# Performance work log

Measured on AMD Instinct MI355X. Metric: run time of the kernel, lower is better.

## Reference

```python
import jax, jax.numpy as jnp
import numpy as np
import math

HID = 512
HEADS = 8
DK = HID // HEADS
B, S, T = 8, 4096, 512


def setup_inputs() -> dict:
    key = jax.random.key(0)
    ks = jax.random.split(key, 12)
    scale = 0.02
    inp = {
        "inputs": jax.random.normal(ks[0], (B, S, HID), dtype=jnp.float32),
        "targets": jax.random.normal(ks[1], (B, T, HID), dtype=jnp.float32),
        "mask": jnp.ones((B, S), dtype=bool),
        "Wq": jax.random.normal(ks[2], (HID, HID), dtype=jnp.float32) * scale,
        "bq": jnp.zeros((HID,), dtype=jnp.float32),
        "Wk": jax.random.normal(ks[3], (HID, HID), dtype=jnp.float32) * scale,
        "bk": jnp.zeros((HID,), dtype=jnp.float32),
        "Wv": jax.random.normal(ks[4], (HID, HID), dtype=jnp.float32) * scale,
        "bv": jnp.zeros((HID,), dtype=jnp.float32),
        "Wo": jax.random.normal(ks[5], (HID, HID), dtype=jnp.float32) * scale,
        "bo": jnp.zeros((HID,), dtype=jnp.float32),
    }
    return inp


def reference(inputs, targets, mask, Wq, bq, Wk, bk, Wv, bv, Wo, bo):
    # PoolingFunction(method='multihead-attention'), dropout=0 (identity),
    # hidden_size == output_size so mapping_function is identity.
    b, t, h = targets.shape
    s = inputs.shape[1]
    Q = (targets @ Wq.T + bq).reshape(b, t, HEADS, DK)
    K = (inputs @ Wk.T + bk).reshape(b, s, HEADS, DK)
    V = (inputs @ Wv.T + bv).reshape(b, s, HEADS, DK)
    # scores: b x heads x tgt x seq (same math as (Q*K).sum(-1)/sqrt(d_k))
    e = jnp.einsum('bthd,bshd->bhts', Q, K) / math.sqrt(DK)
    neg = (1.0 - mask.astype(jnp.float32)) * -1e20  # b x s
    e = e + neg[:, None, None, :]
    a = jax.nn.softmax(e, axis=-1)  # softmax over seq dim
    ctx = jnp.einsum('bhts,bshd->bthd', a, V).reshape(b, t, h)
    return ctx @ Wo.T + bo
```

## Files before the change

### kernel.cpp

```cpp
#include <hip/hip_runtime.h>
#include <hip/hip_bf16.h>
#include <cstdint>
#include <cstddef>

#define HIDN   512
#define NHEADS 8
#define BATCH  8
#define SLEN   4096
#define TLEN   512
#define SSPLIT 4
#define SCHUNK (SLEN / SSPLIT)
#define SCL2   0.18033688f

typedef __attribute__((ext_vector_type(8))) short   bf16x8;
typedef __attribute__((ext_vector_type(4))) float   f32x4;
typedef unsigned short u16;
typedef unsigned int   u32;

__device__ __forceinline__ u32 pkbf(float a, float b) {
    __hip_bfloat162 h = __float22bfloat162_rn(float2{a, b});
    union { __hip_bfloat162 h; u32 u; } un; un.h = h; return un.u;
}
__device__ __forceinline__ u32 cvtpk(float a, float b) {
    u32 r;
    asm("v_cvt_pk_bf16_f32 %0, %1, %2" : "=v"(r) : "v"(a), "v"(b));
    return r;
}
__device__ __forceinline__ float fexp2(float x) {
    return __builtin_amdgcn_exp2f(x);
}
__device__ __forceinline__ void gload_lds16(const u16* g, u16* l) {
    __builtin_amdgcn_global_load_lds(
        (const __attribute__((address_space(1))) u32*)g,
        (__attribute__((address_space(3))) u32*)l, 16, 0, 0);
}

__global__ __launch_bounds__(256) void cvt_all(
    const float* __restrict__ X, const float* __restrict__ Tg,
    const float* __restrict__ Wq, const float* __restrict__ Wk,
    const float* __restrict__ Wv, const float* __restrict__ Wo,
    const int* __restrict__ mask,
    u16* __restrict__ Xc, u16* __restrict__ Tc, u16* __restrict__ Wc,
    float* __restrict__ negf)
{
    int i4 = blockIdx.x * 256 + threadIdx.x;
    if (i4 >= 4980736) {
        int off = i4 - 4980736;
        int4 mv = ((const int4*)mask)[off];
        float4 nv;
        nv.x = mv.x ? 0.f : -1e30f; nv.y = mv.y ? 0.f : -1e30f;
        nv.z = mv.z ? 0.f : -1e30f; nv.w = mv.w ? 0.f : -1e30f;
        ((float4*)negf)[off] = nv;
        return;
    }
    const float* s; u16* d; long off;
    if (i4 < 4194304)      { s = X;  d = Xc; off = i4; }
    else if (i4 < 4718592) { s = Tg; d = Tc; off = i4 - 4194304; }
    else {
        int wi = i4 - 4718592; int widx = wi >> 16;
        s = (widx == 0) ? Wq : (widx == 1) ? Wk : (widx == 2) ? Wv : Wo;
        d = Wc + widx * 262144; off = wi & 65535;
    }
    float4 v = *(const float4*)(s + off * 4);
    uint2 o; o.x = pkbf(v.x, v.y); o.y = pkbf(v.z, v.w);
    *(uint2*)(d + off * 4) = o;
}

#define GEMM_PIPE_DECLS                                                      \
    const int xg = (qd ^ (m & 3)) * 8;                                       \
    const int f0 = tid, f1 = tid + 256;                                      \
    const int r0r = f0 >> 2, r0c = ((f0 & 3) ^ (r0r & 3)) * 8;               \
    const int r1r = f1 >> 2, r1c = ((f1 & 3) ^ (r1r & 3)) * 8;               \
    const int r0b = (f0 & ~63) * 8, r1b = (f1 & ~63) * 8

#define GSTAGE(Aptr, Bptr, k0, bb) do {                                      \
        gload_lds16(Aptr + (size_t)(m0 + r0r) * HIDN + (k0) + r0c,           \
                    &As[bb][0] + r0b);                                       \
        gload_lds16(Bptr + (size_t)(n0 + r0r) * HIDN + (k0) + r0c,           \
                    &Bs[bb][0] + r0b);                                       \
        gload_lds16(Aptr + (size_t)(m0 + r1r) * HIDN + (k0) + r1c,           \
                    &As[bb][0] + r1b);                                       \
        gload_lds16(Bptr + (size_t)(n0 + r1r) * HIDN + (k0) + r1c,           \
                    &Bs[bb][0] + r1b);                                       \
    } while (0)

#define GCOMP(bb) do {                                                       \
        bf16x8 af[4], bf[4];                                                 \
        _Pragma("unroll")                                                    \
        for (int t = 0; t < 4; ++t) {                                        \
            af[t] = *(bf16x8*)&As[bb][(64 * wm + 16 * t + m) * 32 + xg];     \
            bf[t] = *(bf16x8*)&Bs[bb][(64 * wn + 16 * t + m) * 32 + xg];     \
        }                                                                    \
        _Pragma("unroll")                                                    \
        for (int ti = 0; ti < 4; ++ti)                                       \
            _Pragma("unroll")                                                \
            for (int tj = 0; tj < 4; ++tj)                                   \
                acc[ti][tj] = __builtin_amdgcn_mfma_f32_16x16x32_bf16(       \
                    af[ti], bf[tj], acc[ti][tj], 0, 0, 0);                   \
    } while (0)

#define GEMM_PIPE_LOOP(Aptr, Bptr) do {                                      \
        GSTAGE(Aptr, Bptr, 0, 0);                                            \
        _Pragma("unroll 1")                                                  \
        for (int c = 0; c < (HIDN / 32) - 1; ++c) {                          \
            GSTAGE(Aptr, Bptr, (c + 1) * 32, (c + 1) & 1);                   \
            asm volatile("s_waitcnt vmcnt(4)" ::: "memory");                 \
            __builtin_amdgcn_s_barrier();                                    \
            __builtin_amdgcn_sched_barrier(0);                               \
            GCOMP(c & 1);                                                    \
            __builtin_amdgcn_s_barrier();                                    \
            __builtin_amdgcn_sched_barrier(0);                               \
        }                                                                    \
        asm volatile("s_waitcnt vmcnt(0)" ::: "memory");                     \
        __builtin_amdgcn_s_barrier();                                        \
        __builtin_amdgcn_sched_barrier(0);                                   \
        GCOMP(((HIDN / 32) - 1) & 1);                                        \
    } while (0)

template<int MODE, int SEQ>
__global__ __launch_bounds__(256)
void gemm_bf16(const u16* __restrict__ A, const u16* __restrict__ Bw,
               const float* __restrict__ bias, void* __restrict__ Yv)
{
    __shared__ u16 As[2][128 * 32];
    __shared__ u16 Bs[2][128 * 32];
    const int tid = threadIdx.x;
    const int lane = tid & 63, w = tid >> 6;
    const int m = lane & 15, qd = lane >> 4;
    const int wm = w >> 1, wn = w & 1;
    const int m0 = blockIdx.y * 128, n0 = blockIdx.x * 128;
    GEMM_PIPE_DECLS;

    f32x4 acc[4][4];
#pragma unroll
    for (int i = 0; i < 4; ++i)
#pragma unroll
        for (int j = 0; j < 4; ++j) acc[i][j] = (f32x4){0.f, 0.f, 0.f, 0.f};

    GEMM_PIPE_LOOP(A, Bw);

#pragma unroll
    for (int ti = 0; ti < 4; ++ti) {
        const int gr0 = m0 + 64 * wm + 16 * ti + 4 * qd;
#pragma unroll
        for (int tj = 0; tj < 4; ++tj) {
            const int gcol = n0 + 64 * wn + 16 * tj + m;
            const float bv = bias[gcol];
            if (MODE == 0) {
                float* Y = (float*)Yv;
#pragma unroll
                for (int i = 0; i < 4; ++i)
                    Y[(size_t)(gr0 + i) * HIDN + gcol] = acc[ti][tj][i] + bv;
            } else {
                u16* Y = (u16*)Yv;
                const int b = gr0 / SEQ, h = gcol >> 6, d = gcol & 63;
                const int r = gr0 & (SEQ - 1);
                uint2 o;
                o.x = pkbf(acc[ti][tj][0] + bv, acc[ti][tj][1] + bv);
                o.y = pkbf(acc[ti][tj][2] + bv, acc[ti][tj][3] + bv);
                *(uint2*)&Y[(((size_t)(b * 8 + h)) * 64 + d) * SEQ + r] = o;
            }
        }
    }
}

template<int SEQ>
__global__ __launch_bounds__(256)
void gemm_wxT(const u16* __restrict__ Wm, const u16* __restrict__ X,
              const float* __restrict__ bias, u16* __restrict__ Y)
{
    __shared__ u16 As[2][128 * 32];
    __shared__ u16 Bs[2][128 * 32];
    const int tid = threadIdx.x;
    const int lane = tid & 63, w = tid >> 6;
    const int m = lane & 15, qd = lane >> 4;
    const int wm = w >> 1, wn = w & 1;
    const int m0 = blockIdx.y * 128, n0 = blockIdx.x * 128;
    GEMM_PIPE_DECLS;

    f32x4 acc[4][4];
#pragma unroll
    for (int i = 0; i < 4; ++i)
#pragma unroll
        for (int j = 0; j < 4; ++j) acc[i][j] = (f32x4){0.f, 0.f, 0.f, 0.f};

    GEMM_PIPE_LOOP(Wm, X);

#pragma unroll
    for (int ti = 0; ti < 4; ++ti) {
        const int o = m0 + 64 * wm + 16 * ti + 4 * qd;
        const float4 bv = *(const float4*)&bias[o];
        const int h = o >> 6, d0 = o & 63;
#pragma unroll
        for (int tj = 0; tj < 4; ++tj) {
            const int n = n0 + 64 * wn + 16 * tj + m;
            const int b = n / SEQ, r = n & (SEQ - 1);
            uint2 pk;
            pk.x = pkbf(acc[ti][tj][0] + bv.x, acc[ti][tj][1] + bv.y);
            pk.y = pkbf(acc[ti][tj][2] + bv.z, acc[ti][tj][3] + bv.w);
            *(uint2*)&Y[(((size_t)(b * 8 + h)) * SEQ + r) * 64 + d0] = pk;
        }
    }
}

__global__ __launch_bounds__(256, 2)
void attn_part(const u16* __restrict__ Q, const u16* __restrict__ K,
               const u16* __restrict__ Vt, const float* __restrict__ negf,
               float* __restrict__ Opart, float* __restrict__ lpart)
{
    __shared__ char Psh[32768];
    __shared__ u16  KVl[2][8192];
    __shared__ float Ngl[1024];
    const int tid = threadIdx.x;
    const int lane = tid & 63, w = tid >> 6;
    const int m = lane & 15, qd = lane >> 4;
    const int ti = blockIdx.x, si = blockIdx.y, bh = blockIdx.z;
    const int b = bh >> 3;

    const u16* Qp = Q + ((size_t)bh * TLEN + ti * 256) * 64;
    const u16* Kp = K + (size_t)bh * SLEN * 64;
    const u16* Vp = Vt + (size_t)bh * 64 * SLEN;
    const float* np = negf + (size_t)b * SLEN;
    const int s_beg = si * SCHUNK;

    const int sr = tid >> 3;
    const int sg = ((tid & 7) ^ (sr & 7)) * 8;
    const u16* kgb = Kp + (size_t)s_beg * 64 + sr * 64 + sg;
    const u16* vgb = Vp + s_beg + (size_t)sr * SLEN + sg;
    u16* kd = &KVl[0][0]    + tid * 8;
    u16* vd = &KVl[0][4096] + tid * 8;

#define STAGE(cc, bb) do {                                                   \
        const u16* kg_ = kgb + (size_t)(cc) * 4096;                          \
        const u16* vg_ = vgb + (cc) * 64;                                    \
        u16* kd_ = kd + (bb) * 8192;                                         \
        u16* vd_ = vd + (bb) * 8192;                                         \
        gload_lds16(kg_,                     kd_);                           \
        gload_lds16(kg_ + 32 * 64,           kd_ + 2048);                    \
        gload_lds16(vg_,                     vd_);                           \
        gload_lds16(vg_ + (size_t)32 * SLEN, vd_ + 2048);                    \
    } while (0)

    const int wb = w * 8192 + m * 128;
    int waddr[4], ra0[2], ra1[2];
#pragma unroll
    for (int st = 0; st < 4; ++st) waddr[st] = wb + (((4 * st + qd) ^ m) << 3);
#pragma unroll
    for (int ks = 0; ks < 2; ++ks) {
        const int u0 = 8 * ks + 2 * qd;
        ra0[ks] = wb + (((u0) ^ m) << 3);
        ra1[ks] = wb + (((u0 + 1) ^ m) << 3);
    }
    const int x0 = ((qd    ) ^ (m & 7)) * 8;
    const int x1 = ((4 + qd) ^ (m & 7)) * 8;

    bf16x8 qf[4][2];
#pragma unroll
    for (int ts = 0; ts < 4; ++ts)
#pragma unroll
        for (int kh = 0; kh < 2; ++kh)
            qf[ts][kh] = *(const bf16x8*)(Qp + (64 * w + 16 * ts + m) * 64 +
                                          32 * kh + 8 * qd);

    f32x4 O[4][4];
#pragma unroll
    for (int ts = 0; ts < 4; ++ts)
#pragma unroll
        for (int dt = 0; dt < 4; ++dt) O[ts][dt] = (f32x4){0.f, 0.f, 0.f, 0.f};
    float lr[4] = {0.f, 0.f, 0.f, 0.f};

#define CHUNK(cc) do {                                                       \
        const u16* Kl = &KVl[(cc) & 1][0];                                   \
        const u16* Vl = &KVl[(cc) & 1][4096];                                \
        bf16x8 kf[4][2];                                                     \
        _Pragma("unroll")                                                    \
        for (int st = 0; st < 4; ++st) {                                     \
            kf[st][0] = *(const bf16x8*)&Kl[st * 1024 + m * 64 + x0];        \
            kf[st][1] = *(const bf16x8*)&Kl[st * 1024 + m * 64 + x1];        \
        }                                                                    \
        float4 ng[4];                                                        \
        _Pragma("unroll")                                                    \
        for (int st = 0; st < 4; ++st)                                       \
            ng[st] = *(const float4*)&Ngl[((cc) << 6) + (st << 4) + (qd << 2)]; \
        _Pragma("unroll")                                                    \
        for (int ts = 0; ts < 4; ++ts) {                                     \
            f32x4 S[4];                                                      \
            _Pragma("unroll")                                                \
            for (int st = 0; st < 4; ++st) {                                 \
                f32x4 cc2 = (f32x4){0.f, 0.f, 0.f, 0.f};                     \
                cc2 = __builtin_amdgcn_mfma_f32_16x16x32_bf16(               \
                          kf[st][0], qf[ts][0], cc2, 0, 0, 0);               \
                cc2 = __builtin_amdgcn_mfma_f32_16x16x32_bf16(               \
                          kf[st][1], qf[ts][1], cc2, 0, 0, 0);               \
                S[st] = cc2;                                                 \
            }                                                                \
            float ls = 0.f;                                                  \
            _Pragma("unroll")                                                \
            for (int st = 0; st < 4; ++st) {                                 \
                const float p0 = fexp2(fmaf(S[st][0], SCL2, ng[st].x));      \
                const float p1 = fexp2(fmaf(S[st][1], SCL2, ng[st].y));      \
                const float p2 = fexp2(fmaf(S[st][2], SCL2, ng[st].z));      \
                const float p3 = fexp2(fmaf(S[st][3], SCL2, ng[st].w));      \
                ls += (p0 + p1) + (p2 + p3);                                 \
                *(uint2*)&Psh[waddr[st] + ts * 2048] =                       \
                    make_uint2(cvtpk(p0, p1), cvtpk(p2, p3));                \
            }                                                                \
            lr[ts] += ls;                                                    \
        }                                                                    \
        bf16x8 vf[4][2];                                                     \
        _Pragma("unroll")                                                    \
        for (int dt = 0; dt < 4; ++dt) {                                     \
            vf[dt][0] = *(const bf16x8*)&Vl[dt * 1024 + m * 64 + x0];        \
            vf[dt][1] = *(const bf16x8*)&Vl[dt * 1024 + m * 64 + x1];        \
        }                                                                    \
        __builtin_amdgcn_s_setprio(1);                                       \
        _Pragma("unroll")                                                    \
        for (int ts = 0; ts < 4; ++ts) {                                     \
            _Pragma("unroll")                                                \
            for (int ks = 0; ks < 2; ++ks) {                                 \
                const uint2 r0 = *(uint2*)&Psh[ra0[ks] + ts * 2048];         \
                const uint2 r1 = *(uint2*)&Psh[ra1[ks] + ts * 2048];         \
                union { uint4 u; bf16x8 v; } bu;                             \
                bu.u = make_uint4(r0.x, r0.y, r1.x, r1.y);                   \
                O[ts][0] = __builtin_amdgcn_mfma_f32_16x16x32_bf16(          \
                               vf[0][ks], bu.v, O[ts][0], 0, 0, 0);          \
                O[ts][1] = __builtin_amdgcn_mfma_f32_16x16x32_bf16(          \
                               vf[1][ks], bu.v, O[ts][1], 0, 0, 0);          \
                O[ts][2] = __builtin_amdgcn_mfma_f32_16x16x32_bf16(          \
                               vf[2][ks], bu.v, O[ts][2], 0, 0, 0);          \
                O[ts][3] = __builtin_amdgcn_mfma_f32_16x16x32_bf16(          \
                               vf[3][ks], bu.v, O[ts][3], 0, 0, 0);          \
            }                                                                \
        }                                                                    \
        __builtin_amdgcn_s_setprio(0);                                       \
    } while (0)

    STAGE(0, 0);
    gload_lds16((const u16*)(np + s_beg) + (size_t)tid * 8,
                ((u16*)Ngl) + tid * 8);
#pragma unroll 1
    for (int c = 0; c < (SCHUNK / 64) - 1; ++c) {
        STAGE(c + 1, (c + 1) & 1);
        asm volatile("s_waitcnt vmcnt(4)" ::: "memory");
        __builtin_amdgcn_s_barrier();
        __builtin_amdgcn_sched_barrier(0);
        CHUNK(c);
        __builtin_amdgcn_s_barrier();
        __builtin_amdgcn_sched_barrier(0);
    }
    asm volatile("s_waitcnt vmcnt(0)" ::: "memory");
    __builtin_amdgcn_s_barrier();
    __builtin_amdgcn_sched_barrier(0);
    CHUNK((SCHUNK / 64) - 1);

#undef STAGE
#undef CHUNK

#pragma unroll
    for (int ts = 0; ts < 4; ++ts) {
        float l = lr[ts];
        l += __shfl_xor(l, 16, 64);
        l += __shfl_xor(l, 32, 64);
        const int t = ti * 256 + 64 * w + 16 * ts + m;
        float* Ob = Opart + (((size_t)(si * 64 + bh)) * 512 + t) * 64;
#pragma unroll
        for (int dt = 0; dt < 4; ++dt)
            *(f32x4*)&Ob[16 * dt + 4 * qd] = O[ts][dt];
        if (qd == 0)
            lpart[((size_t)(si * 64 + bh)) * 512 + t] = l;
    }
}

__global__ __launch_bounds__(256)
void attn_combine(const float* __restrict__ Opart, const float* __restrict__ lpart,
                  u16* __restrict__ ctx)
{
    const int gid = blockIdx.x * 256 + threadIdx.x;
    const int d4 = gid & 15, t = (gid >> 4) & 511, bh = gid >> 13;
    const int b = bh >> 3, h = bh & 7;
    float4 o = {0.f, 0.f, 0.f, 0.f}; float l = 0.f;
#pragma unroll
    for (int si = 0; si < SSPLIT; ++si) {
        const size_t base = ((size_t)(si * 64 + bh)) * 512 + t;
        l += lpart[base];
        const float4 v = *(const float4*)(Opart + base * 64 + d4 * 4);
        o.x += v.x; o.y += v.y; o.z += v.z; o.w += v.w;
    }
    const float r = 1.f / l;
    uint2 pk; pk.x = pkbf(o.x * r, o.y * r); pk.y = pkbf(o.z * r, o.w * r);
    *(uint2*)&ctx[((size_t)(b * 512 + t)) * 512 + h * 64 + d4 * 4] = pk;
}

extern "C" void kernel_launch(void* const* d_in, const int* in_sizes, int n_in,
                              void* d_out, int out_size, void* d_ws, size_t ws_size,
                              hipStream_t stream)
{
    const float* inputs  = (const float*)d_in[0];
    const float* targets = (const float*)d_in[1];
    const int*   mask    = (const int*)d_in[2];
    const float* Wq = (const float*)d_in[3];
    const float* bq = (const float*)d_in[4];
    const float* Wk = (const float*)d_in[5];
    const float* bk = (const float*)d_in[6];
    const float* Wv = (const float*)d_in[7];
    const float* bv = (const float*)d_in[8];
    const float* Wo = (const float*)d_in[9];
    const float* bo = (const float*)d_in[10];

    char* ws = (char*)d_ws;
    u16*   Xc    = (u16*)(ws);
    u16*   Tc    = (u16*)(ws + 33554432);
    u16*   Wc    = (u16*)(ws + 37748736);
    float* negf  = (float*)(ws + 39845888);
    u16*   Qws   = (u16*)(ws + 39976960);
    u16*   Kws   = (u16*)(ws + 44171264);
    u16*   Vtws  = (u16*)(ws + 77725696);
    u16*   Cws   = (u16*)(ws + 111280128);
    float* Opart = (float*)(ws + 115474432);
    float* lpart = (float*)(ws + 149028864);

    cvt_all<<<19488, 256, 0, stream>>>(inputs, targets, Wq, Wk, Wv, Wo, mask,
                                       Xc, Tc, Wc, negf);

    gemm_wxT<TLEN><<<dim3(32, 4),  256, 0, stream>>>(Wc,          Tc, bq, Qws);
    gemm_wxT<SLEN><<<dim3(256, 4), 256, 0, stream>>>(Wc + 262144, Xc, bk, Kws);
    gemm_bf16<2, SLEN><<<dim3(4, 256), 256, 0, stream>>>(Xc, Wc + 524288, bv, Vtws);

    attn_part<<<dim3(2, SSPLIT, 64), 256, 0, stream>>>(Qws, Kws, Vtws, negf,
                                                       Opart, lpart);
    attn_combine<<<2048, 256, 0, stream>>>(Opart, lpart, Cws);

    gemm_bf16<0, TLEN><<<dim3(4, 32), 256, 0, stream>>>(Cws, Wc + 786432, bo,
                                                        (float*)d_out);
}
```

Before: 279.4 us.

## Fuse Q/K/V projections into one launch and use triple-buffered GEMM ring

Replaces the double-buffered GEMM main loop with a three-stage LDS ring that keeps two k-chunks of global-to-LDS loads in flight. Merges the Q, K and V projection GEMMs into a single kernel that dispatches on block index, removing two launches and the tail idle between them. LDS per block grows to 48KB, which may reduce occupancy, and the loop is fully unrolled, which increases code size.

```diff
diff --git a/kernel.cpp b/kernel.cpp
--- a/kernel.cpp
+++ b/kernel.cpp
@@ -66,14 +66,14 @@
     *(uint2*)(d + off * 4) = o;
 }
 
-#define GEMM_PIPE_DECLS                                                      \
-    const int xg = (qd ^ (m & 3)) * 8;                                       \
-    const int f0 = tid, f1 = tid + 256;                                      \
-    const int r0r = f0 >> 2, r0c = ((f0 & 3) ^ (r0r & 3)) * 8;               \
-    const int r1r = f1 >> 2, r1c = ((f1 & 3) ^ (r1r & 3)) * 8;               \
-    const int r0b = (f0 & ~63) * 8, r1b = (f1 & ~63) * 8
-
-#define GSTAGE(Aptr, Bptr, k0, bb) do {                                      \
+
+#define GEMM_RING_DECLS                                                      \
+    const int xg  = (qd ^ (m & 3)) * 8;                                      \
+    const int r0r = tid >> 2,         r0c = ((tid & 3) ^ (r0r & 3)) * 8;     \
+    const int r1r = (tid + 256) >> 2, r1c = ((tid & 3) ^ (r1r & 3)) * 8;     \
+    const int r0b = (tid & ~63) * 8,  r1b = ((tid + 256) & ~63) * 8
+
+#define PSTG(Aptr, Bptr, bb, k0) do {                                        \
         gload_lds16(Aptr + (size_t)(m0 + r0r) * HIDN + (k0) + r0c,           \
                     &As[bb][0] + r0b);                                       \
         gload_lds16(Bptr + (size_t)(n0 + r0r) * HIDN + (k0) + r0c,           \
@@ -84,7 +84,7 @@
                     &Bs[bb][0] + r1b);                                       \
     } while (0)
 
-#define GCOMP(bb) do {                                                       \
+#define PCMP(bb) do {                                                        \
         bf16x8 af[4], bf[4];                                                 \
         _Pragma("unroll")                                                    \
         for (int t = 0; t < 4; ++t) {                                        \
@@ -99,37 +99,43 @@
                     af[ti], bf[tj], acc[ti][tj], 0, 0, 0);                   \
     } while (0)
 
-#define GEMM_PIPE_LOOP(Aptr, Bptr) do {                                      \
-        GSTAGE(Aptr, Bptr, 0, 0);                                            \
-        _Pragma("unroll 1")                                                  \
-        for (int c = 0; c < (HIDN / 32) - 1; ++c) {                          \
-            GSTAGE(Aptr, Bptr, (c + 1) * 32, (c + 1) & 1);                   \
-            asm volatile("s_waitcnt vmcnt(4)" ::: "memory");                 \
+#define WAIT_BAR(N) do {                                                     \
+        asm volatile("s_waitcnt vmcnt(" #N ")" ::: "memory");                \
+        __builtin_amdgcn_s_barrier();                                        \
+        __builtin_amdgcn_sched_barrier(0);                                   \
+    } while (0)
+
+#define GEMM_RING_LOOP(Aptr, Bptr) do {                                      \
+        PSTG(Aptr, Bptr, 0, 0);                                              \
+        PSTG(Aptr, Bptr, 1, 32);                                             \
+        _Pragma("unroll")                                                    \
+        for (int c = 0; c < 14; ++c) {                                       \
+            PSTG(Aptr, Bptr, (c + 2) % 3, (c + 2) * 32);                     \
+            WAIT_BAR(8);                                                     \
+            PCMP(c % 3);                                                     \
             __builtin_amdgcn_s_barrier();                                    \
             __builtin_amdgcn_sched_barrier(0);                               \
-            GCOMP(c & 1);                                                    \
-            __builtin_amdgcn_s_barrier();                                    \
-            __builtin_amdgcn_sched_barrier(0);                               \
-        }                                                                    \
-        asm volatile("s_waitcnt vmcnt(0)" ::: "memory");                     \
+        }                                                                    \
+        WAIT_BAR(4);                                                         \
+        PCMP(2);                                                   \
         __builtin_amdgcn_s_barrier();                                        \
         __builtin_amdgcn_sched_barrier(0);                                   \
-        GCOMP(((HIDN / 32) - 1) & 1);                                        \
+        WAIT_BAR(0);                                                         \
+        PCMP(0);                                                   \
     } while (0)
 
 template<int MODE, int SEQ>
-__global__ __launch_bounds__(256)
-void gemm_bf16(const u16* __restrict__ A, const u16* __restrict__ Bw,
-               const float* __restrict__ bias, void* __restrict__ Yv)
-{
-    __shared__ u16 As[2][128 * 32];
-    __shared__ u16 Bs[2][128 * 32];
+__device__ __forceinline__ void gemmA_body(
+    const u16* __restrict__ A, const u16* __restrict__ Bw,
+    const float* __restrict__ bias, void* __restrict__ Yv,
+    int m0, int n0, u16 (*As)[4096], u16 (*Bs)[4096])
+{
     const int tid = threadIdx.x;
-    const int lane = tid & 63, w = tid >> 6;
+    const int lane = tid & 63;
+    const int w = tid >> 6;
     const int m = lane & 15, qd = lane >> 4;
     const int wm = w >> 1, wn = w & 1;
-    const int m0 = blockIdx.y * 128, n0 = blockIdx.x * 128;
-    GEMM_PIPE_DECLS;
+    GEMM_RING_DECLS;
 
     f32x4 acc[4][4];
 #pragma unroll
@@ -137,7 +143,7 @@
 #pragma unroll
         for (int j = 0; j < 4; ++j) acc[i][j] = (f32x4){0.f, 0.f, 0.f, 0.f};
 
-    GEMM_PIPE_LOOP(A, Bw);
+    GEMM_RING_LOOP(A, Bw);
 
 #pragma unroll
     for (int ti = 0; ti < 4; ++ti) {
@@ -165,18 +171,17 @@
 }
 
 template<int SEQ>
-__global__ __launch_bounds__(256)
-void gemm_wxT(const u16* __restrict__ Wm, const u16* __restrict__ X,
-              const float* __restrict__ bias, u16* __restrict__ Y)
-{
-    __shared__ u16 As[2][128 * 32];
-    __shared__ u16 Bs[2][128 * 32];
+__device__ __forceinline__ void wxT_body(
+    const u16* __restrict__ Wm, const u16* __restrict__ X,
+    const float* __restrict__ bias, u16* __restrict__ Y,
+    int m0, int n0, u16 (*As)[4096], u16 (*Bs)[4096])
+{
     const int tid = threadIdx.x;
-    const int lane = tid & 63, w = tid >> 6;
+    const int lane = tid & 63;
+    const int w = tid >> 6;
     const int m = lane & 15, qd = lane >> 4;
     const int wm = w >> 1, wn = w & 1;
-    const int m0 = blockIdx.y * 128, n0 = blockIdx.x * 128;
-    GEMM_PIPE_DECLS;
+    GEMM_RING_DECLS;
 
     f32x4 acc[4][4];
 #pragma unroll
@@ -184,7 +189,7 @@
 #pragma unroll
         for (int j = 0; j < 4; ++j) acc[i][j] = (f32x4){0.f, 0.f, 0.f, 0.f};
 
-    GEMM_PIPE_LOOP(Wm, X);
+    GEMM_RING_LOOP(Wm, X);
 
 #pragma unroll
     for (int ti = 0; ti < 4; ++ti) {
@@ -201,6 +206,41 @@
             *(uint2*)&Y[(((size_t)(b * 8 + h)) * SEQ + r) * 64 + d0] = pk;
         }
     }
+}
+
+__global__ __launch_bounds__(256)
+void proj_all(const u16* __restrict__ Wc, const u16* __restrict__ Tc,
+              const u16* __restrict__ Xc,
+              const float* __restrict__ bq, const float* __restrict__ bk,
+              const float* __restrict__ bv,
+              u16* __restrict__ Qws, u16* __restrict__ Kws,
+              u16* __restrict__ Vtws)
+{
+    __shared__ u16 As[3][4096];
+    __shared__ u16 Bs[3][4096];
+    const int bid = blockIdx.x;
+    if (bid < 1024) {
+        wxT_body<SLEN>(Wc + 262144, Xc, bk, Kws,
+                       (bid >> 8) * 128, (bid & 255) * 128, As, Bs);
+    } else if (bid < 2048) {
+        const int b2 = bid - 1024;
+        gemmA_body<2, SLEN>(Xc, Wc + 524288, bv, Vtws,
+                            (b2 >> 2) * 128, (b2 & 3) * 128, As, Bs);
+    } else {
+        const int b2 = bid - 2048;
+        wxT_body<TLEN>(Wc, Tc, bq, Qws,
+                       (b2 >> 5) * 128, (b2 & 31) * 128, As, Bs);
+    }
+}
+
+__global__ __launch_bounds__(256)
+void gemm_out(const u16* __restrict__ A, const u16* __restrict__ Bw,
+              const float* __restrict__ bias, float* __restrict__ Y)
+{
+    __shared__ u16 As[3][4096];
+    __shared__ u16 Bs[3][4096];
+    gemmA_body<0, TLEN>(A, Bw, bias, Y,
+                        blockIdx.y * 128, blockIdx.x * 128, As, Bs);
 }
 
 __global__ __launch_bounds__(256, 2)
@@ -422,14 +462,13 @@
     cvt_all<<<19488, 256, 0, stream>>>(inputs, targets, Wq, Wk, Wv, Wo, mask,
                                        Xc, Tc, Wc, negf);
 
-    gemm_wxT<TLEN><<<dim3(32, 4),  256, 0, stream>>>(Wc,          Tc, bq, Qws);
-    gemm_wxT<SLEN><<<dim3(256, 4), 256, 0, stream>>>(Wc + 262144, Xc, bk, Kws);
-    gemm_bf16<2, SLEN><<<dim3(4, 256), 256, 0, stream>>>(Xc, Wc + 524288, bv, Vtws);
+    proj_all<<<2176, 256, 0, stream>>>(Wc, Tc, Xc, bq, bk, bv,
+                                       Qws, Kws, Vtws);
 
     attn_part<<<dim3(2, SSPLIT, 64), 256, 0, stream>>>(Qws, Kws, Vtws, negf,
                                                        Opart, lpart);
     attn_combine<<<2048, 256, 0, stream>>>(Opart, lpart, Cws);
 
-    gemm_bf16<0, TLEN><<<dim3(4, 32), 256, 0, stream>>>(Cws, Wc + 786432, bo,
-                                                        (float*)d_out);
-}
+    gemm_out<<<dim3(4, 32), 256, 0, stream>>>(Cws, Wc + 786432, bo,
+                                              (float*)d_out);
+}
```

Result: faster. 258.6 us (-7.4%).
